# Performance work log

Hardware: AMD Instinct MI355X
Metric: run time of the kernel (lower is better)

The kernel has to match this reference:

```python
import jax, jax.numpy as jnp
import numpy as np
from jax import lax

ALPHA = 0.1  # leak rate


def setup_inputs() -> dict:
    key = jax.random.key(0)
    ks = jax.random.split(key, 6)
    B, T, I, H, O = 64, 512, 128, 512, 64
    # Weights scaled by 1/sqrt(fan_in) for numerical sanity (torch code uses raw randn,
    # which saturates tanh immediately; math is identical, only init scale differs).
    return {
        "inputs": jax.random.normal(ks[0], (B, T, I), dtype=jnp.float32),
        "hidden": jnp.zeros((B, H), dtype=jnp.float32),
        "W_in": jax.random.normal(ks[1], (H, I), dtype=jnp.float32) / np.sqrt(I),
        "W_rec": jax.random.normal(ks[2], (H, H), dtype=jnp.float32) / np.sqrt(H),
        "b": jax.random.normal(ks[3], (H,), dtype=jnp.float32),
        "W_out": jax.random.normal(ks[4], (O, H), dtype=jnp.float32) / np.sqrt(H),
        "b_out": jax.random.normal(ks[5], (O,), dtype=jnp.float32),
    }


def reference(inputs, hidden, W_in, W_rec, b, W_out, b_out):
    # inputs: [B,T,I], hidden: [B,H]
    # Precompute input projections for all timesteps in one GEMM: [B,T,H]
    x_proj = jnp.einsum('bti,hi->bth', inputs, W_in)

    def step(h, xp_t):  # h: [B,H], xp_t: [B,H]
        pre = xp_t + jnp.einsum('bj,hj->bh', h, W_rec) + b
        h_new = (1.0 - ALPHA) * h + ALPHA * jnp.tanh(pre)
        out_t = jnp.einsum('bh,oh->bo', h_new, W_out) + b_out
        return h_new, out_t

    h_final, outs = lax.scan(step, hidden, jnp.swapaxes(x_proj, 0, 1))  # outs: [T,B,O]
    return jnp.swapaxes(outs, 0, 1), h_final  # ([B,T,O], [B,H])
```

## Files before the change

kernel.cpp:

```cpp
#include <hip/hip_runtime.h>
#include <stdint.h>

#define B_ 64
#define T_ 512
#define I_ 128
#define H_ 512
#define O_ 64
#define ALPHA_ 0.1f

typedef _Float16 f16;
typedef _Float16 f16x2 __attribute__((ext_vector_type(2)));

__device__ __forceinline__ uint32_t pkf16(float a, float b) {
  f16 ha = (f16)a, hb = (f16)b;
  uint16_t ua = __builtin_bit_cast(uint16_t, ha);
  uint16_t ub = __builtin_bit_cast(uint16_t, hb);
  return (uint32_t)ua | ((uint32_t)ub << 16);
}

__device__ __forceinline__ float dot2(uint32_t w, uint32_t h, float acc) {
#if __has_builtin(__builtin_amdgcn_fdot2)
  return __builtin_amdgcn_fdot2(__builtin_bit_cast(f16x2, w),
                                __builtin_bit_cast(f16x2, h), acc, false);
#else
  f16x2 wv = __builtin_bit_cast(f16x2, w), hv = __builtin_bit_cast(f16x2, h);
  return acc + (float)wv[0] * (float)hv[0] + (float)wv[1] * (float)hv[1];
#endif
}

__device__ __forceinline__ float tanhfast(float x) {
  float e = __expf(2.0f * x);
#if __has_builtin(__builtin_amdgcn_rcpf)
  return 1.0f - 2.0f * __builtin_amdgcn_rcpf(e + 1.0f);
#else
  return 1.0f - 2.0f / (e + 1.0f);
#endif
}

__global__ __launch_bounds__(256) void pack_w(
    const float* __restrict__ Wrec, const float* __restrict__ Win,
    const float* __restrict__ Wout, uint32_t* __restrict__ wrecT,
    uint32_t* __restrict__ winT, uint32_t* __restrict__ woutT) {
  int id = blockIdx.x * 256 + threadIdx.x;
  if (id < 512 * 256) {
    int t = id >> 8, k = id & 255;
    const float* s = Wrec + t * 512 + 2 * k;
    wrecT[k * 512 + t] = pkf16(s[0], s[1]);
  } else if (id < 512 * 256 + 512 * 64) {
    int j = id - 512 * 256;
    int n = j >> 6, k = j & 63;
    const float* s = Win + n * 128 + 2 * k;
    winT[k * 512 + n] = pkf16(s[0], s[1]);
  } else {
    int j = id - (512 * 256 + 512 * 64);
    int o = j >> 8, k = j & 255;
    const float* s = Wout + o * 512 + 2 * k;
    woutT[k * 64 + o] = pkf16(s[0], s[1]);
  }
}

__global__ __launch_bounds__(512) void xproj_k(
    const float* __restrict__ in, const uint32_t* __restrict__ winT,
    f16* __restrict__ xp) {
  __shared__ uint32_t A[32][64];
  const int t = threadIdx.x;
  const int m0 = blockIdx.x * 32;
#pragma unroll
  for (int i = 0; i < 4; i++) {
    int id = i * 512 + t;
    int r = id >> 6, k = id & 63;
    const float* s = in + (m0 + r) * I_ + 2 * k;
    A[r][k] = pkf16(s[0], s[1]);
  }
  uint32_t w[64];
#pragma unroll
  for (int k = 0; k < 64; k++) w[k] = winT[k * 512 + t];
  __syncthreads();
  for (int r = 0; r < 32; r++) {
    float a0 = 0.f, a1 = 0.f, a2 = 0.f, a3 = 0.f;
#pragma unroll
    for (int k4 = 0; k4 < 16; k4++) {
      uint4 hq = *((const uint4*)&A[r][k4 * 4]);
      a0 = dot2(w[4 * k4 + 0], hq.x, a0);
      a1 = dot2(w[4 * k4 + 1], hq.y, a1);
      a2 = dot2(w[4 * k4 + 2], hq.z, a2);
      a3 = dot2(w[4 * k4 + 3], hq.w, a3);
    }
    xp[(m0 + r) * H_ + t] = (f16)((a0 + a1) + (a2 + a3));
  }
}

#define NV 192
#define NL 64
__global__ __attribute__((amdgpu_flat_work_group_size(512, 512),
                          amdgpu_waves_per_eu(2, 2)))
void rnn_k(const uint32_t* __restrict__ wrecT, const f16* __restrict__ xp,
           const float* __restrict__ bias, const float* __restrict__ h0,
           f16* __restrict__ hall, float* __restrict__ hfin) {
  extern __shared__ uint32_t lds[];
  uint32_t* hbuf = lds;
  uint4* wldsQ = (uint4*)(lds + 512);
  const int b = blockIdx.x, t = threadIdx.x;

  uint32_t w[NV];
#pragma unroll
  for (int k = 0; k < NV; k++) w[k] = wrecT[k * 512 + t];
#pragma unroll
  for (int q = 0; q < NL / 4; q++) {
    uint4 v;
    v.x = wrecT[(NV + 4 * q + 0) * 512 + t];
    v.y = wrecT[(NV + 4 * q + 1) * 512 + t];
    v.z = wrecT[(NV + 4 * q + 2) * 512 + t];
    v.w = wrecT[(NV + 4 * q + 3) * 512 + t];
    wldsQ[q * 512 + t] = v;
  }

  float hv = h0[b * H_ + t];
  const float bia = bias[t];
  ((f16*)hbuf)[t] = (f16)hv;

  const f16* xpp = xp + b * (T_ * H_) + t;
  f16* hap = hall + b * H_ + t;
  float xv = (float)xpp[0];
  __syncthreads();

  for (int ts = 0; ts < T_; ++ts) {
    float xn = 0.f;
    if (ts + 1 < T_) xn = (float)xpp[(ts + 1) * H_];
    const uint32_t* hb = hbuf + (ts & 1) * 256;
    float a0 = 0.f, a1 = 0.f, a2 = 0.f, a3 = 0.f;
#pragma unroll
    for (int k4 = 0; k4 < NV / 4; k4++) {
      uint4 hq = *((const uint4*)(hb + 4 * k4));
      a0 = dot2(w[4 * k4 + 0], hq.x, a0);
      a1 = dot2(w[4 * k4 + 1], hq.y, a1);
      a2 = dot2(w[4 * k4 + 2], hq.z, a2);
      a3 = dot2(w[4 * k4 + 3], hq.w, a3);
    }
#pragma unroll
    for (int q = 0; q < NL / 4; q++) {
      uint4 wq = wldsQ[q * 512 + t];
      uint4 hq = *((const uint4*)(hb + NV + 4 * q));
      a0 = dot2(wq.x, hq.x, a0);
      a1 = dot2(wq.y, hq.y, a1);
      a2 = dot2(wq.z, hq.z, a2);
      a3 = dot2(wq.w, hq.w, a3);
    }
    float pre = ((a0 + a1) + (a2 + a3)) + bia + xv;
    hv = (1.0f - ALPHA_) * hv + ALPHA_ * tanhfast(pre);
    f16 hh = (f16)hv;
    ((f16*)hbuf)[(((ts + 1) & 1) << 9) + t] = hh;
    hap[ts * (B_ * H_)] = hh;
    xv = xn;
    asm volatile("s_waitcnt lgkmcnt(0)" ::: "memory");
    __builtin_amdgcn_s_barrier();
    asm volatile("" ::: "memory");
  }
  hfin[b * H_ + t] = hv;
}

__global__ __launch_bounds__(256) void outgemm_k(
    const f16* __restrict__ hall, const uint32_t* __restrict__ woutT,
    const float* __restrict__ bout, float* __restrict__ out) {
  __shared__ uint32_t A[32][256];
  const int bid = blockIdx.x;
  const int b = bid >> 4, ts0 = (bid & 15) * 32;
  const int t = threadIdx.x, o = t & 63, g = t >> 6;
  const uint32_t* hp = (const uint32_t*)hall;
#pragma unroll
  for (int i = 0; i < 32; i++) {
    int id = i * 256 + t;
    int r = id >> 8, k = id & 255;
    A[r][k] = hp[(ts0 + r) * (B_ * H_ / 2) + b * (H_ / 2) + k];
  }
  const float bo = bout[o];
  __syncthreads();
  float acc[8];
#pragma unroll
  for (int r = 0; r < 8; r++) acc[r] = 0.f;
  for (int k4 = 0; k4 < 64; k4++) {
    uint32_t w0 = woutT[(4 * k4 + 0) * 64 + o];
    uint32_t w1 = woutT[(4 * k4 + 1) * 64 + o];
    uint32_t w2 = woutT[(4 * k4 + 2) * 64 + o];
    uint32_t w3 = woutT[(4 * k4 + 3) * 64 + o];
#pragma unroll
    for (int r = 0; r < 8; r++) {
      uint4 hq = *((const uint4*)&A[g * 8 + r][k4 * 4]);
      acc[r] = dot2(w0, hq.x, acc[r]);
      acc[r] = dot2(w1, hq.y, acc[r]);
      acc[r] = dot2(w2, hq.z, acc[r]);
      acc[r] = dot2(w3, hq.w, acc[r]);
    }
  }
#pragma unroll
  for (int r = 0; r < 8; r++)
    out[(b * T_ + ts0 + g * 8 + r) * O_ + o] = acc[r] + bo;
}

extern "C" void kernel_launch(void* const* d_in, const int* in_sizes, int n_in,
                              void* d_out, int out_size, void* d_ws,
                              size_t ws_size, hipStream_t stream) {
  const float* inputs = (const float*)d_in[0];
  const float* h0     = (const float*)d_in[1];
  const float* Win    = (const float*)d_in[2];
  const float* Wrec   = (const float*)d_in[3];
  const float* bias   = (const float*)d_in[4];
  const float* Wout   = (const float*)d_in[5];
  const float* bout   = (const float*)d_in[6];
  float* out = (float*)d_out;

  uint8_t* ws = (uint8_t*)d_ws;
  uint32_t* wrecT = (uint32_t*)(ws);
  uint32_t* winT  = (uint32_t*)(ws + (512u << 10));
  uint32_t* woutT = (uint32_t*)(ws + (640u << 10));
  f16* xp   = (f16*)(ws + (1u << 20));
  f16* hall = (f16*)(ws + (1u << 20) + (32u << 20));

  hipLaunchKernelGGL(pack_w, dim3(704), dim3(256), 0, stream, Wrec, Win, Wout,
                     wrecT, winT, woutT);
  hipLaunchKernelGGL(xproj_k, dim3(32768 / 32), dim3(512), 0, stream, inputs,
                     winT, xp);
  const int rnn_lds = (512 + (NL / 4) * 512 * 4) * 4;
  hipFuncSetAttribute((const void*)rnn_k,
                      hipFuncAttributeMaxDynamicSharedMemorySize, rnn_lds);
  hipLaunchKernelGGL(rnn_k, dim3(B_), dim3(512), rnn_lds, stream, wrecT, xp,
                     bias, h0, hall, out + B_ * T_ * O_);
  hipLaunchKernelGGL(outgemm_k, dim3(B_ * (T_ / 32)), dim3(256), 0, stream,
                     hall, woutT, bout, out);
}
```

Measured before the change: 839.0 us.

## Split recurrent h reads between LDS and global memory across thread halves

Threads 256-511 of the recurrent kernel now read the previous hidden state from the global hall buffer (or from a new f16 copy of h0 at the first step), while threads 0-255 keep reading it from LDS. The aim is to halve LDS read bandwidth per step. The change also moves more W_rec columns into registers (224 instead of 192) and fewer into LDS, and pads dynamic LDS to 96 KB. In exchange it puts cache-latency global loads on the serial per-step critical path, relies on intra-block global visibility after __syncthreads, and raises register pressure, with a risk of spills.

```diff
diff --git a/kernel.cpp b/kernel.cpp
--- a/kernel.cpp
+++ b/kernel.cpp
@@ -90,13 +90,14 @@
   }
 }
 
-#define NV 192
-#define NL 64
+#define NV 224
+#define NL 32
 __global__ __attribute__((amdgpu_flat_work_group_size(512, 512),
                           amdgpu_waves_per_eu(2, 2)))
 void rnn_k(const uint32_t* __restrict__ wrecT, const f16* __restrict__ xp,
            const float* __restrict__ bias, const float* __restrict__ h0,
-           f16* __restrict__ hall, float* __restrict__ hfin) {
+           f16* __restrict__ h0h, f16* __restrict__ hall,
+           float* __restrict__ hfin) {
   extern __shared__ uint32_t lds[];
   uint32_t* hbuf = lds;
   uint4* wldsQ = (uint4*)(lds + 512);
@@ -117,7 +118,9 @@
 
   float hv = h0[b * H_ + t];
   const float bia = bias[t];
-  ((f16*)hbuf)[t] = (f16)hv;
+  f16 hini = (f16)hv;
+  ((f16*)hbuf)[t] = hini;
+  h0h[b * H_ + t] = hini;
 
   const f16* xpp = xp + b * (T_ * H_) + t;
   f16* hap = hall + b * H_ + t;
@@ -127,24 +130,48 @@
   for (int ts = 0; ts < T_; ++ts) {
     float xn = 0.f;
     if (ts + 1 < T_) xn = (float)xpp[(ts + 1) * H_];
-    const uint32_t* hb = hbuf + (ts & 1) * 256;
     float a0 = 0.f, a1 = 0.f, a2 = 0.f, a3 = 0.f;
-#pragma unroll
-    for (int k4 = 0; k4 < NV / 4; k4++) {
-      uint4 hq = *((const uint4*)(hb + 4 * k4));
-      a0 = dot2(w[4 * k4 + 0], hq.x, a0);
-      a1 = dot2(w[4 * k4 + 1], hq.y, a1);
-      a2 = dot2(w[4 * k4 + 2], hq.z, a2);
-      a3 = dot2(w[4 * k4 + 3], hq.w, a3);
-    }
-#pragma unroll
-    for (int q = 0; q < NL / 4; q++) {
-      uint4 wq = wldsQ[q * 512 + t];
-      uint4 hq = *((const uint4*)(hb + NV + 4 * q));
-      a0 = dot2(wq.x, hq.x, a0);
-      a1 = dot2(wq.y, hq.y, a1);
-      a2 = dot2(wq.z, hq.z, a2);
-      a3 = dot2(wq.w, hq.w, a3);
+    if (t < 256) {
+      const uint4* hq4 = (const uint4*)(hbuf + (ts & 1) * 256);
+#pragma unroll
+      for (int k4 = 0; k4 < NV / 4; k4++) {
+        uint4 hq = hq4[k4];
+        a0 = dot2(w[4 * k4 + 0], hq.x, a0);
+        a1 = dot2(w[4 * k4 + 1], hq.y, a1);
+        a2 = dot2(w[4 * k4 + 2], hq.z, a2);
+        a3 = dot2(w[4 * k4 + 3], hq.w, a3);
+      }
+#pragma unroll
+      for (int q = 0; q < NL / 4; q++) {
+        uint4 wq = wldsQ[q * 512 + t];
+        uint4 hq = hq4[NV / 4 + q];
+        a0 = dot2(wq.x, hq.x, a0);
+        a1 = dot2(wq.y, hq.y, a1);
+        a2 = dot2(wq.z, hq.z, a2);
+        a3 = dot2(wq.w, hq.w, a3);
+      }
+    } else {
+      const uint4* hg =
+          (ts == 0) ? (const uint4*)(h0h + b * H_)
+                    : (const uint4*)(hall + (size_t)(ts - 1) * (B_ * H_) +
+                                     b * H_);
+#pragma unroll
+      for (int k4 = 0; k4 < NV / 4; k4++) {
+        uint4 hq = hg[k4];
+        a0 = dot2(w[4 * k4 + 0], hq.x, a0);
+        a1 = dot2(w[4 * k4 + 1], hq.y, a1);
+        a2 = dot2(w[4 * k4 + 2], hq.z, a2);
+        a3 = dot2(w[4 * k4 + 3], hq.w, a3);
+      }
+#pragma unroll
+      for (int q = 0; q < NL / 4; q++) {
+        uint4 wq = wldsQ[q * 512 + t];
+        uint4 hq = hg[NV / 4 + q];
+        a0 = dot2(wq.x, hq.x, a0);
+        a1 = dot2(wq.y, hq.y, a1);
+        a2 = dot2(wq.z, hq.z, a2);
+        a3 = dot2(wq.w, hq.w, a3);
+      }
     }
     float pre = ((a0 + a1) + (a2 + a3)) + bia + xv;
     hv = (1.0f - ALPHA_) * hv + ALPHA_ * tanhfast(pre);
@@ -152,9 +179,7 @@
     ((f16*)hbuf)[(((ts + 1) & 1) << 9) + t] = hh;
     hap[ts * (B_ * H_)] = hh;
     xv = xn;
-    asm volatile("s_waitcnt lgkmcnt(0)" ::: "memory");
-    __builtin_amdgcn_s_barrier();
-    asm volatile("" ::: "memory");
+    __syncthreads();
   }
   hfin[b * H_ + t] = hv;
 }
@@ -213,6 +238,7 @@
   uint32_t* wrecT = (uint32_t*)(ws);
   uint32_t* winT  = (uint32_t*)(ws + (512u << 10));
   uint32_t* woutT = (uint32_t*)(ws + (640u << 10));
+  f16* h0h  = (f16*)(ws + (704u << 10));
   f16* xp   = (f16*)(ws + (1u << 20));
   f16* hall = (f16*)(ws + (1u << 20) + (32u << 20));
 
@@ -220,11 +246,11 @@
                      wrecT, winT, woutT);
   hipLaunchKernelGGL(xproj_k, dim3(32768 / 32), dim3(512), 0, stream, inputs,
                      winT, xp);
-  const int rnn_lds = (512 + (NL / 4) * 512 * 4) * 4;
+  const int rnn_lds = 98304;
   hipFuncSetAttribute((const void*)rnn_k,
                       hipFuncAttributeMaxDynamicSharedMemorySize, rnn_lds);
   hipLaunchKernelGGL(rnn_k, dim3(B_), dim3(512), rnn_lds, stream, wrecT, xp,
-                     bias, h0, hall, out + B_ * T_ * O_);
+                     bias, h0, h0h, hall, out + B_ * T_ * O_);
   hipLaunchKernelGGL(outgemm_k, dim3(B_ * (T_ / 32)), dim3(256), 0, stream,
                      hall, woutT, bout, out);
 }
```

Measured after the change: 2.372 ms. +182.7%, slower.

## Split recurrent matvec by K across waves with LDS partial-sum reduction

Applied to the files above, without the earlier changes.

Restructures the recurrent step so each wave owns a 64-wide slice of the hidden input and computes partial dot products for 8 output rows per lane. This cuts LDS broadcast reads of h per thread. The remaining weights, previously held in LDS, are now streamed from global/L2 every timestep in two phases. Partials are written to LDS and summed across 8 waves after the barrier. The cost is per-step global weight traffic, an extra LDS reduction, and a more complex pack layout.

```diff
diff --git a/kernel.cpp b/kernel.cpp
--- a/kernel.cpp
+++ b/kernel.cpp
@@ -7,6 +7,12 @@
 #define H_ 512
 #define O_ 64
 #define ALPHA_ 0.1f
+
+#define CV 22
+#define CS 10
+#define R_END (176 * 512)
+#define S_END (R_END + 80 * 512)
+#define WIN_END (S_END + 512 * 64)
 
 typedef _Float16 f16;
 typedef _Float16 f16x2 __attribute__((ext_vector_type(2)));
@@ -39,21 +45,31 @@
 
 __global__ __launch_bounds__(256) void pack_w(
     const float* __restrict__ Wrec, const float* __restrict__ Win,
-    const float* __restrict__ Wout, uint32_t* __restrict__ wrecT,
-    uint32_t* __restrict__ winT, uint32_t* __restrict__ woutT) {
+    const float* __restrict__ Wout, uint32_t* __restrict__ wrecR,
+    uint32_t* __restrict__ wrecS, uint32_t* __restrict__ winT,
+    uint32_t* __restrict__ woutT) {
   int id = blockIdx.x * 256 + threadIdx.x;
-  if (id < 512 * 256) {
-    int t = id >> 8, k = id & 255;
-    const float* s = Wrec + t * 512 + 2 * k;
-    wrecT[k * 512 + t] = pkf16(s[0], s[1]);
-  } else if (id < 512 * 256 + 512 * 64) {
-    int j = id - 512 * 256;
-    int n = j >> 6, k = j & 63;
+  if (id < R_END) {
+    int cj = id >> 9, t = id & 511;
+    int j = cj / CV, c = cj % CV;
+    int row = 64 * j + (t & 63), col = 64 * (t >> 6) + 2 * c;
+    const float* s = Wrec + row * 512 + col;
+    wrecR[id] = pkf16(s[0], s[1]);
+  } else if (id < S_END) {
+    int e = id - R_END;
+    int g = e >> 11, rem = e & 2047, t = rem >> 2, q = rem & 3;
+    int i70 = g * 4 + q, j = i70 / CS, cc = i70 % CS;
+    int row = 64 * j + (t & 63), col = 64 * (t >> 6) + 2 * (CV + cc);
+    const float* s = Wrec + row * 512 + col;
+    wrecS[e] = pkf16(s[0], s[1]);
+  } else if (id < WIN_END) {
+    int e = id - S_END;
+    int n = e >> 6, k = e & 63;
     const float* s = Win + n * 128 + 2 * k;
     winT[k * 512 + n] = pkf16(s[0], s[1]);
   } else {
-    int j = id - (512 * 256 + 512 * 64);
-    int o = j >> 8, k = j & 255;
+    int e = id - WIN_END;
+    int o = e >> 8, k = e & 255;
     const float* s = Wout + o * 512 + 2 * k;
     woutT[k * 64 + o] = pkf16(s[0], s[1]);
   }
@@ -90,30 +106,22 @@
   }
 }
 
-#define NV 192
-#define NL 64
 __global__ __attribute__((amdgpu_flat_work_group_size(512, 512),
                           amdgpu_waves_per_eu(2, 2)))
-void rnn_k(const uint32_t* __restrict__ wrecT, const f16* __restrict__ xp,
-           const float* __restrict__ bias, const float* __restrict__ h0,
-           f16* __restrict__ hall, float* __restrict__ hfin) {
-  extern __shared__ uint32_t lds[];
-  uint32_t* hbuf = lds;
-  uint4* wldsQ = (uint4*)(lds + 512);
+void rnn_k(const uint32_t* __restrict__ wrecR, const uint32_t* __restrict__ wrecS,
+           const f16* __restrict__ xp, const float* __restrict__ bias,
+           const float* __restrict__ h0, f16* __restrict__ hall,
+           float* __restrict__ hfin) {
+  __shared__ uint32_t hbuf[512];
+  __shared__ float pld[8 * 512];
   const int b = blockIdx.x, t = threadIdx.x;
-
-  uint32_t w[NV];
-#pragma unroll
-  for (int k = 0; k < NV; k++) w[k] = wrecT[k * 512 + t];
-#pragma unroll
-  for (int q = 0; q < NL / 4; q++) {
-    uint4 v;
-    v.x = wrecT[(NV + 4 * q + 0) * 512 + t];
-    v.y = wrecT[(NV + 4 * q + 1) * 512 + t];
-    v.z = wrecT[(NV + 4 * q + 2) * 512 + t];
-    v.w = wrecT[(NV + 4 * q + 3) * 512 + t];
-    wldsQ[q * 512 + t] = v;
-  }
+  const int l = t & 63, wv = t >> 6;
+
+  uint32_t wr[8][CV];
+#pragma unroll
+  for (int j = 0; j < 8; j++)
+#pragma unroll
+    for (int c = 0; c < CV; c++) wr[j][c] = wrecR[(j * CV + c) * 512 + t];
 
   float hv = h0[b * H_ + t];
   const float bia = bias[t];
@@ -121,32 +129,75 @@
 
   const f16* xpp = xp + b * (T_ * H_) + t;
   f16* hap = hall + b * H_ + t;
+  const uint4* sQ = (const uint4*)wrecS;
   float xv = (float)xpp[0];
   __syncthreads();
 
   for (int ts = 0; ts < T_; ++ts) {
+    uint32_t s0v[40];
+#pragma unroll
+    for (int g = 0; g < 10; g++) {
+      uint4 v = sQ[g * 512 + t];
+      s0v[4 * g + 0] = v.x; s0v[4 * g + 1] = v.y;
+      s0v[4 * g + 2] = v.z; s0v[4 * g + 3] = v.w;
+    }
+    __builtin_amdgcn_sched_barrier(0);
+    const uint32_t* hb = hbuf + ((ts & 1) << 8) + (wv << 5);
+    float acc[8];
+#pragma unroll
+    for (int j = 0; j < 8; j++) acc[j] = 0.f;
+#pragma unroll
+    for (int qd = 0; qd < 5; qd++) {
+      uint4 q = *((const uint4*)(hb + 4 * qd));
+      uint32_t qa[4] = {q.x, q.y, q.z, q.w};
+#pragma unroll
+      for (int cc = 0; cc < 4; cc++)
+#pragma unroll
+        for (int j = 0; j < 8; j++)
+          acc[j] = dot2(wr[j][qd * 4 + cc], qa[cc], acc[j]);
+    }
+    uint4 q5 = *((const uint4*)(hb + 20));
+    uint4 q6 = *((const uint4*)(hb + 24));
+    uint4 q7 = *((const uint4*)(hb + 28));
+#pragma unroll
+    for (int j = 0; j < 8; j++) {
+      acc[j] = dot2(wr[j][20], q5.x, acc[j]);
+      acc[j] = dot2(wr[j][21], q5.y, acc[j]);
+    }
+    uint32_t hs[10] = {q5.z, q5.w, q6.x, q6.y, q6.z,
+                       q6.w, q7.x, q7.y, q7.z, q7.w};
+#pragma unroll
+    for (int j = 0; j < 4; j++)
+#pragma unroll
+      for (int cc = 0; cc < CS; cc++)
+        acc[j] = dot2(s0v[j * CS + cc], hs[cc], acc[j]);
+    __builtin_amdgcn_sched_barrier(0);
+    uint32_t s1v[40];
+#pragma unroll
+    for (int g = 0; g < 10; g++) {
+      uint4 v = sQ[(10 + g) * 512 + t];
+      s1v[4 * g + 0] = v.x; s1v[4 * g + 1] = v.y;
+      s1v[4 * g + 2] = v.z; s1v[4 * g + 3] = v.w;
+    }
+    __builtin_amdgcn_sched_barrier(0);
+#pragma unroll
+    for (int j = 0; j < 4; j++) pld[(wv << 9) + (j << 6) + l] = acc[j];
+#pragma unroll
+    for (int j = 4; j < 8; j++)
+#pragma unroll
+      for (int cc = 0; cc < CS; cc++)
+        acc[j] = dot2(s1v[(j - 4) * CS + cc], hs[cc], acc[j]);
+#pragma unroll
+    for (int j = 4; j < 8; j++) pld[(wv << 9) + (j << 6) + l] = acc[j];
     float xn = 0.f;
     if (ts + 1 < T_) xn = (float)xpp[(ts + 1) * H_];
-    const uint32_t* hb = hbuf + (ts & 1) * 256;
-    float a0 = 0.f, a1 = 0.f, a2 = 0.f, a3 = 0.f;
-#pragma unroll
-    for (int k4 = 0; k4 < NV / 4; k4++) {
-      uint4 hq = *((const uint4*)(hb + 4 * k4));
-      a0 = dot2(w[4 * k4 + 0], hq.x, a0);
-      a1 = dot2(w[4 * k4 + 1], hq.y, a1);
-      a2 = dot2(w[4 * k4 + 2], hq.z, a2);
-      a3 = dot2(w[4 * k4 + 3], hq.w, a3);
-    }
-#pragma unroll
-    for (int q = 0; q < NL / 4; q++) {
-      uint4 wq = wldsQ[q * 512 + t];
-      uint4 hq = *((const uint4*)(hb + NV + 4 * q));
-      a0 = dot2(wq.x, hq.x, a0);
-      a1 = dot2(wq.y, hq.y, a1);
-      a2 = dot2(wq.z, hq.z, a2);
-      a3 = dot2(wq.w, hq.w, a3);
-    }
-    float pre = ((a0 + a1) + (a2 + a3)) + bia + xv;
+    asm volatile("s_waitcnt lgkmcnt(0)" ::: "memory");
+    __builtin_amdgcn_s_barrier();
+    asm volatile("" ::: "memory");
+    float sum = 0.f;
+#pragma unroll
+    for (int w8 = 0; w8 < 8; w8++) sum += pld[(w8 << 9) + t];
+    float pre = sum + bia + xv;
     hv = (1.0f - ALPHA_) * hv + ALPHA_ * tanhfast(pre);
     f16 hh = (f16)hv;
     ((f16*)hbuf)[(((ts + 1) & 1) << 9) + t] = hh;
@@ -210,20 +261,18 @@
   float* out = (float*)d_out;
 
   uint8_t* ws = (uint8_t*)d_ws;
-  uint32_t* wrecT = (uint32_t*)(ws);
-  uint32_t* winT  = (uint32_t*)(ws + (512u << 10));
-  uint32_t* woutT = (uint32_t*)(ws + (640u << 10));
+  uint32_t* wrecR = (uint32_t*)(ws);
+  uint32_t* wrecS = (uint32_t*)(ws + (384u << 10));
+  uint32_t* winT  = (uint32_t*)(ws + (576u << 10));
+  uint32_t* woutT = (uint32_t*)(ws + (704u << 10));
   f16* xp   = (f16*)(ws + (1u << 20));
   f16* hall = (f16*)(ws + (1u << 20) + (32u << 20));
 
   hipLaunchKernelGGL(pack_w, dim3(704), dim3(256), 0, stream, Wrec, Win, Wout,
-                     wrecT, winT, woutT);
+                     wrecR, wrecS, winT, woutT);
   hipLaunchKernelGGL(xproj_k, dim3(32768 / 32), dim3(512), 0, stream, inputs,
                      winT, xp);
-  const int rnn_lds = (512 + (NL / 4) * 512 * 4) * 4;
-  hipFuncSetAttribute((const void*)rnn_k,
-                      hipFuncAttributeMaxDynamicSharedMemorySize, rnn_lds);
-  hipLaunchKernelGGL(rnn_k, dim3(B_), dim3(512), rnn_lds, stream, wrecT, xp,
+  hipLaunchKernelGGL(rnn_k, dim3(B_), dim3(512), 0, stream, wrecR, wrecS, xp,
                      bias, h0, hall, out + B_ * T_ * O_);
   hipLaunchKernelGGL(outgemm_k, dim3(B_ * (T_ / 32)), dim3(256), 0, stream,
                      hall, woutT, bout, out);
```

Measured after the change: 2.232 ms. 2.66x slower.

## Split recurrent matvec over K across waves with LDS partial-sum reduction

Applied to the files above, without the earlier changes.

Each wave now owns a 64-column slice of the hidden state and computes partial dot products for 8 row blocks. The recurrent weights are repacked into a matching register-plus-LDS layout. Partial sums go to LDS and are reduced per row after a barrier. The aim is to cut per-thread LDS reads of the hidden vector from 256 dwords to 32 per timestep. The cost is an extra barrier per step, extra LDS partial-sum traffic, and a single-buffered h that now relies on two barriers.

```diff
diff --git a/kernel.cpp b/kernel.cpp
--- a/kernel.cpp
+++ b/kernel.cpp
@@ -7,6 +7,12 @@
 #define H_ 512
 #define O_ 64
 #define ALPHA_ 0.1f
+
+#define NV 24
+#define R_DW (192 * 512)
+#define L_END (R_DW + 64 * 512)
+#define WIN_END (L_END + 512 * 64)
+#define WOUT_END (WIN_END + 64 * 256)
 
 typedef _Float16 f16;
 typedef _Float16 f16x2 __attribute__((ext_vector_type(2)));
@@ -37,23 +43,39 @@
 #endif
 }
 
+#define DOT4S(A, S, HQ)                                             \
+  A = dot2((S).w, (HQ).w,                                           \
+      dot2((S).z, (HQ).z, dot2((S).y, (HQ).y, dot2((S).x, (HQ).x, A))))
+
 __global__ __launch_bounds__(256) void pack_w(
     const float* __restrict__ Wrec, const float* __restrict__ Win,
-    const float* __restrict__ Wout, uint32_t* __restrict__ wrecT,
-    uint32_t* __restrict__ winT, uint32_t* __restrict__ woutT) {
+    const float* __restrict__ Wout, uint32_t* __restrict__ wrecR,
+    uint32_t* __restrict__ wrecL, uint32_t* __restrict__ winT,
+    uint32_t* __restrict__ woutT) {
   int id = blockIdx.x * 256 + threadIdx.x;
-  if (id < 512 * 256) {
-    int t = id >> 8, k = id & 255;
-    const float* s = Wrec + t * 512 + 2 * k;
-    wrecT[k * 512 + t] = pkf16(s[0], s[1]);
-  } else if (id < 512 * 256 + 512 * 64) {
-    int j = id - 512 * 256;
-    int n = j >> 6, k = j & 63;
+  if (id < R_DW) {
+    int t = id & 511, cj = id >> 9;
+    int j = cj / NV, c = cj % NV;
+    int row = 64 * j + (t & 63), col = 64 * (t >> 6) + 2 * c;
+    const float* s = Wrec + row * 512 + col;
+    wrecR[id] = pkf16(s[0], s[1]);
+  } else if (id < L_END) {
+    int e = id - R_DW;
+    int comp = e & 3, i4 = e >> 2;
+    int t = i4 & 511, qj = i4 >> 9;
+    int j = qj >> 1, qq = qj & 1;
+    int row = 64 * j + (t & 63);
+    int col = 64 * (t >> 6) + 2 * (NV + 4 * qq + comp);
+    const float* s = Wrec + row * 512 + col;
+    wrecL[e] = pkf16(s[0], s[1]);
+  } else if (id < WIN_END) {
+    int e = id - L_END;
+    int n = e >> 6, k = e & 63;
     const float* s = Win + n * 128 + 2 * k;
     winT[k * 512 + n] = pkf16(s[0], s[1]);
   } else {
-    int j = id - (512 * 256 + 512 * 64);
-    int o = j >> 8, k = j & 255;
+    int e = id - WIN_END;
+    int o = e >> 8, k = e & 255;
     const float* s = Wout + o * 512 + 2 * k;
     woutT[k * 64 + o] = pkf16(s[0], s[1]);
   }
@@ -90,30 +112,26 @@
   }
 }
 
-#define NV 192
-#define NL 64
 __global__ __attribute__((amdgpu_flat_work_group_size(512, 512),
                           amdgpu_waves_per_eu(2, 2)))
-void rnn_k(const uint32_t* __restrict__ wrecT, const f16* __restrict__ xp,
-           const float* __restrict__ bias, const float* __restrict__ h0,
-           f16* __restrict__ hall, float* __restrict__ hfin) {
+void rnn_k(const uint32_t* __restrict__ wrecR, const uint4* __restrict__ wrecL4,
+           const f16* __restrict__ xp, const float* __restrict__ bias,
+           const float* __restrict__ h0, f16* __restrict__ hall,
+           float* __restrict__ hfin) {
   extern __shared__ uint32_t lds[];
   uint32_t* hbuf = lds;
-  uint4* wldsQ = (uint4*)(lds + 512);
+  float* pld = (float*)(lds + 256);
+  uint4* wq = (uint4*)(lds + 256 + 4096);
   const int b = blockIdx.x, t = threadIdx.x;
-
-  uint32_t w[NV];
-#pragma unroll
-  for (int k = 0; k < NV; k++) w[k] = wrecT[k * 512 + t];
-#pragma unroll
-  for (int q = 0; q < NL / 4; q++) {
-    uint4 v;
-    v.x = wrecT[(NV + 4 * q + 0) * 512 + t];
-    v.y = wrecT[(NV + 4 * q + 1) * 512 + t];
-    v.z = wrecT[(NV + 4 * q + 2) * 512 + t];
-    v.w = wrecT[(NV + 4 * q + 3) * 512 + t];
-    wldsQ[q * 512 + t] = v;
-  }
+  const int l = t & 63, wv = t >> 6;
+
+  uint32_t wr[8][NV];
+#pragma unroll
+  for (int j = 0; j < 8; j++)
+#pragma unroll
+    for (int c = 0; c < NV; c++) wr[j][c] = wrecR[(j * NV + c) * 512 + t];
+#pragma unroll
+  for (int k = 0; k < 16; k++) wq[k * 512 + t] = wrecL4[k * 512 + t];
 
   float hv = h0[b * H_ + t];
   const float bia = bias[t];
@@ -122,34 +140,49 @@
   const f16* xpp = xp + b * (T_ * H_) + t;
   f16* hap = hall + b * H_ + t;
   float xv = (float)xpp[0];
+  const uint32_t* hqb = hbuf + (wv << 5);
   __syncthreads();
 
   for (int ts = 0; ts < T_; ++ts) {
+    float acc[8];
+#pragma unroll
+    for (int j = 0; j < 8; j++) acc[j] = 0.f;
+#pragma unroll
+    for (int q = 0; q < 6; q++) {
+      uint4 hq = *((const uint4*)(hqb + 4 * q));
+#pragma unroll
+      for (int j = 0; j < 8; j++)
+        acc[j] = dot2(wr[j][4 * q + 3], hq.w,
+                 dot2(wr[j][4 * q + 2], hq.z,
+                 dot2(wr[j][4 * q + 1], hq.y,
+                 dot2(wr[j][4 * q + 0], hq.x, acc[j]))));
+    }
+    {
+      uint4 hq6 = *((const uint4*)(hqb + 24));
+      uint4 hq7 = *((const uint4*)(hqb + 28));
+#pragma unroll
+      for (int j = 0; j < 8; j++) {
+        uint4 w6 = wq[(2 * j + 0) * 512 + t];
+        DOT4S(acc[j], w6, hq6);
+        uint4 w7 = wq[(2 * j + 1) * 512 + t];
+        DOT4S(acc[j], w7, hq7);
+      }
+    }
+#pragma unroll
+    for (int j = 0; j < 8; j++) pld[(wv << 9) + (j << 6) + l] = acc[j];
     float xn = 0.f;
     if (ts + 1 < T_) xn = (float)xpp[(ts + 1) * H_];
-    const uint32_t* hb = hbuf + (ts & 1) * 256;
-    float a0 = 0.f, a1 = 0.f, a2 = 0.f, a3 = 0.f;
-#pragma unroll
-    for (int k4 = 0; k4 < NV / 4; k4++) {
-      uint4 hq = *((const uint4*)(hb + 4 * k4));
-      a0 = dot2(w[4 * k4 + 0], hq.x, a0);
-      a1 = dot2(w[4 * k4 + 1], hq.y, a1);
-      a2 = dot2(w[4 * k4 + 2], hq.z, a2);
-      a3 = dot2(w[4 * k4 + 3], hq.w, a3);
-    }
-#pragma unroll
-    for (int q = 0; q < NL / 4; q++) {
-      uint4 wq = wldsQ[q * 512 + t];
-      uint4 hq = *((const uint4*)(hb + NV + 4 * q));
-      a0 = dot2(wq.x, hq.x, a0);
-      a1 = dot2(wq.y, hq.y, a1);
-      a2 = dot2(wq.z, hq.z, a2);
-      a3 = dot2(wq.w, hq.w, a3);
-    }
-    float pre = ((a0 + a1) + (a2 + a3)) + bia + xv;
+    asm volatile("s_waitcnt lgkmcnt(0)" ::: "memory");
+    __builtin_amdgcn_s_barrier();
+    asm volatile("" ::: "memory");
+    float s01 = pld[(0 << 9) + t] + pld[(1 << 9) + t];
+    float s23 = pld[(2 << 9) + t] + pld[(3 << 9) + t];
+    float s45 = pld[(4 << 9) + t] + pld[(5 << 9) + t];
+    float s67 = pld[(6 << 9) + t] + pld[(7 << 9) + t];
+    float pre = ((s01 + s23) + (s45 + s67)) + bia + xv;
     hv = (1.0f - ALPHA_) * hv + ALPHA_ * tanhfast(pre);
     f16 hh = (f16)hv;
-    ((f16*)hbuf)[(((ts + 1) & 1) << 9) + t] = hh;
+    ((f16*)hbuf)[t] = hh;
     hap[ts * (B_ * H_)] = hh;
     xv = xn;
     asm volatile("s_waitcnt lgkmcnt(0)" ::: "memory");
@@ -210,21 +243,23 @@
   float* out = (float*)d_out;
 
   uint8_t* ws = (uint8_t*)d_ws;
-  uint32_t* wrecT = (uint32_t*)(ws);
+  uint32_t* wrecR = (uint32_t*)(ws);
+  uint32_t* wrecL = (uint32_t*)(ws + (384u << 10));
   uint32_t* winT  = (uint32_t*)(ws + (512u << 10));
   uint32_t* woutT = (uint32_t*)(ws + (640u << 10));
   f16* xp   = (f16*)(ws + (1u << 20));
   f16* hall = (f16*)(ws + (1u << 20) + (32u << 20));
 
   hipLaunchKernelGGL(pack_w, dim3(704), dim3(256), 0, stream, Wrec, Win, Wout,
-                     wrecT, winT, woutT);
+                     wrecR, wrecL, winT, woutT);
   hipLaunchKernelGGL(xproj_k, dim3(32768 / 32), dim3(512), 0, stream, inputs,
                      winT, xp);
-  const int rnn_lds = (512 + (NL / 4) * 512 * 4) * 4;
+  const int rnn_lds = 1024 + 16384 + 131072;
   hipFuncSetAttribute((const void*)rnn_k,
                       hipFuncAttributeMaxDynamicSharedMemorySize, rnn_lds);
-  hipLaunchKernelGGL(rnn_k, dim3(B_), dim3(512), rnn_lds, stream, wrecT, xp,
-                     bias, h0, hall, out + B_ * T_ * O_);
+  hipLaunchKernelGGL(rnn_k, dim3(B_), dim3(512), rnn_lds, stream, wrecR,
+                     (const uint4*)wrecL, xp, bias, h0, hall,
+                     out + B_ * T_ * O_);
   hipLaunchKernelGGL(outgemm_k, dim3(B_ * (T_ / 32)), dim3(256), 0, stream,
                      hall, woutT, bout, out);
 }
```

Result: slower. 1.026 ms (+22.3%).
